# Kernel optimization log

Measured on AMD Instinct MI355X. Metric: run time of the kernel, lower is better.

The kernel has to match this reference:

```python
import jax, jax.numpy as jnp
import numpy as np

R0 = 1.0
N_NODES = 10000
N_EDGES = 160000
DIM_A, DIM_V, DIM_D, CHAN = 64, 32, 16, 16

# Levi-Civita tensor for the antisymmetric (cross-product-like) products
_EPS = np.zeros((3, 3, 3), dtype=np.float32)
for (i, j, k), s in (((0,1,2),1.),((1,2,0),1.),((2,0,1),1.),((0,2,1),-1.),((2,1,0),-1.),((1,0,2),-1.)):
    _EPS[i, j, k] = s


def _tl(W, x):
    """TensLinear: mix channel axis 1 of x (B, din, *(3,)*rank) with W (dout, din)."""
    y = jnp.tensordot(x, W, axes=((1,), (1,)))  # (B, *(3,)*rank, dout)
    return jnp.moveaxis(y, -1, 1)


def radial_encode_8(r, r0):
    # 8 Gaussian radial basis functions on |r|/r0
    d = jnp.linalg.norm(r, axis=-1)            # (E,)
    x = d * (8.0 / r0)
    mu = jnp.arange(8, dtype=r.dtype)
    return jnp.exp(-0.5 * (x[:, None] - mu[None, :]) ** 2)  # (E, 8)


def tens_sigmoid_1(v):
    # equivariant squashing: scale vector by tanh(|v|)/|v|
    n = jnp.linalg.norm(v, axis=-1, keepdims=True)
    return v * jnp.tanh(n) / (n + 1e-12)


def _forward(floats, src, dst, n_nodes):
    (r_ij, x_a, x_v, x_d, W_L0, W_L1, W_L2,
     W_Y000, W_Y110, W_Y220, W_Y011, W_Y101, W_Y121, W_Y211,
     W_Y022, W_Y202, W_Y112, W_Y222, W_Y111, W_Y212,
     W_enc, b_enc, W_dir, W1, b1, W2, b2, W3, b3) = floats
    eps = jnp.asarray(_EPS)
    rad = radial_encode_8(r_ij, R0) @ W_enc.T + b_enc        # (E, chan)
    r = tens_sigmoid_1(r_ij * (7.0 / R0))                    # (E, 3)
    phi_a = rad                                              # (E, chan)
    phi_v = rad[:, :, None] * r[:, None, :]                  # (E, chan, 3)
    phi_d = rad[:, :, None, None] * r[:, None, None, :] * r[:, None, :, None]  # (E, chan, 3, 3)
    # gather destination-node features per edge
    x_a_j = _tl(W_L0, x_a)[dst]                              # (E, chan)
    x_v_j = _tl(W_L1, x_v)[dst]                              # (E, chan, 3)
    x_d_j = _tl(W_L2, x_d)[dst]                              # (E, chan, 3, 3)
    # equivariant tensor products (Bee.apply)
    y_000 = x_a_j * phi_a
    y_110 = jnp.sum(x_v_j * phi_v, -1)
    y_220 = jnp.sum(x_d_j * phi_d, (-2, -1))
    y_011 = x_a_j[..., None] * phi_v
    y_101 = x_v_j * phi_a[..., None]
    y_121 = jnp.einsum('ecj,ecji->eci', x_v_j, phi_d)
    y_211 = jnp.einsum('ecij,ecj->eci', x_d_j, phi_v)
    y_022 = x_a_j[..., None, None] * phi_d
    y_202 = x_d_j * phi_a[..., None, None]
    y_112 = x_v_j[..., :, None] * phi_v[..., None, :]
    y_222 = jnp.einsum('ecik,eckj->ecij', x_d_j, phi_d)
    y_111 = jnp.cross(x_v_j, phi_v)
    y_212 = jnp.einsum('ikl,eckj,ecl->ecij', eps, x_d_j, phi_v)
    psi_a = _tl(W_Y000, y_000) + _tl(W_Y110, y_110) + _tl(W_Y220, y_220)
    psi_v = (_tl(W_Y011, y_011) + _tl(W_Y101, y_101) + _tl(W_Y121, y_121)
             + _tl(W_Y211, y_211) + _tl(W_Y111, y_111))
    psi_d = (_tl(W_Y022, y_022) + _tl(W_Y202, y_202) + _tl(W_Y112, y_112)
             + _tl(W_Y222, y_222) + _tl(W_Y212, y_212))
    # residual MLP on the scalar channel: lin_direct(x) + layers(x)
    lrelu = lambda x: jnp.where(x >= 0, x, 0.1 * x)
    h = lrelu(psi_a @ W1.T + b1)
    h = lrelu(h @ W2.T + b2)
    psi_a = psi_a + psi_a @ W_dir.T + (h @ W3.T + b3)
    # scatter-reduce messages to source nodes
    B_a = jax.ops.segment_sum(psi_a, src, num_segments=n_nodes)
    B_v = jax.ops.segment_sum(psi_v, src, num_segments=n_nodes)
    B_d = jax.ops.segment_sum(psi_d, src, num_segments=n_nodes)
    return 0.1 * B_a, 0.1 * B_v, 0.1 * B_d


def setup_inputs() -> dict:
    key = jax.random.key(0)
    ks = jax.random.split(key, 32)
    f32 = jnp.float32
    nrm = lambda k, shape, scale=1.0: scale * jax.random.normal(k, shape, dtype=f32)
    E, N = N_EDGES, N_NODES
    sC = CHAN ** -0.5
    inp = {
        'r_ij': nrm(ks[0], (E, 3)),
        'x_a': nrm(ks[1], (N, DIM_A)),
        'x_v': nrm(ks[2], (N, DIM_V, 3)),
        'x_d': nrm(ks[3], (N, DIM_D, 3, 3)),
        'W_L0': nrm(ks[4], (CHAN, DIM_A), DIM_A ** -0.5),
        'W_L1': nrm(ks[5], (CHAN, DIM_V), DIM_V ** -0.5),
        'W_L2': nrm(ks[6], (CHAN, DIM_D), DIM_D ** -0.5),
        'W_Y000': nrm(ks[7], (DIM_A, CHAN), sC),
        'W_Y110': nrm(ks[8], (DIM_A, CHAN), sC),
        'W_Y220': nrm(ks[9], (DIM_A, CHAN), sC),
        'W_Y011': nrm(ks[10], (DIM_V, CHAN), sC),
        'W_Y101': nrm(ks[11], (DIM_V, CHAN), sC),
        'W_Y121': nrm(ks[12], (DIM_V, CHAN), sC),
        'W_Y211': nrm(ks[13], (DIM_V, CHAN), sC),
        'W_Y022': nrm(ks[14], (DIM_D, CHAN), sC),
        'W_Y202': nrm(ks[15], (DIM_D, CHAN), sC),
        'W_Y112': nrm(ks[16], (DIM_D, CHAN), sC),
        'W_Y222': nrm(ks[17], (DIM_D, CHAN), sC),
        'W_Y111': nrm(ks[18], (DIM_V, CHAN), sC),
        'W_Y212': nrm(ks[19], (DIM_D, CHAN), sC),
        'W_enc': nrm(ks[20], (CHAN, 8), 8 ** -0.5),
        'b_enc': jnp.zeros((CHAN,), f32),
        'W_dir': nrm(ks[21], (DIM_A, DIM_A), DIM_A ** -0.5),
        'W1': nrm(ks[22], (2 * DIM_A, DIM_A), DIM_A ** -0.5),
        'b1': jnp.zeros((2 * DIM_A,), f32),
        'W2': nrm(ks[23], (2 * DIM_A, 2 * DIM_A), (2 * DIM_A) ** -0.5),
        'b2': jnp.zeros((2 * DIM_A,), f32),
        'W3': nrm(ks[24], (DIM_A, 2 * DIM_A), (2 * DIM_A) ** -0.5),
        'b3': jnp.zeros((DIM_A,), f32),
        'src': jax.random.randint(ks[25], (E,), 0, N, dtype=jnp.int32),
        'dst': jax.random.randint(ks[26], (E,), 0, N, dtype=jnp.int32),
        'n_nodes': N,
    }
    return inp


def reference(r_ij, x_a, x_v, x_d, W_L0, W_L1, W_L2, W_Y000, W_Y110, W_Y220,
              W_Y011, W_Y101, W_Y121, W_Y211, W_Y022, W_Y202, W_Y112, W_Y222,
              W_Y111, W_Y212, W_enc, b_enc, W_dir, W1, b1, W2, b2, W3, b3,
              src, dst, n_nodes):
    floats = (r_ij, x_a, x_v, x_d, W_L0, W_L1, W_L2, W_Y000, W_Y110, W_Y220,
              W_Y011, W_Y101, W_Y121, W_Y211, W_Y022, W_Y202, W_Y112, W_Y222,
              W_Y111, W_Y212, W_enc, b_enc, W_dir, W1, b1, W2, b2, W3, b3)
    return _forward(floats, src, dst, n_nodes)
```

## Files before the change

kernel.cpp:

```cpp
#include <hip/hip_runtime.h>
#include <hip/hip_bf16.h>

typedef __hip_bfloat16 bf16;
typedef __attribute__((ext_vector_type(8))) short bf16x8;
typedef __attribute__((ext_vector_type(4))) float f32x4;

__device__ __forceinline__ void st_bf16(short* p, float v) {
    uint32_t u = __float_as_uint(v) + 0x8000u;
    *p = (short)(u >> 16);
}
__device__ __forceinline__ float bb2f(short s) {
    uint32_t u = ((uint32_t)(uint16_t)s) << 16;
    return __uint_as_float(u);
}

__global__ __launch_bounds__(256) void prep_all(
    const float* __restrict__ W000, const float* __restrict__ W110, const float* __restrict__ W220,
    const float* __restrict__ W011, const float* __restrict__ W101, const float* __restrict__ W121,
    const float* __restrict__ W211, const float* __restrict__ W111,
    const float* __restrict__ W022, const float* __restrict__ W202, const float* __restrict__ W112,
    const float* __restrict__ W222, const float* __restrict__ W212,
    const float* __restrict__ W1, const float* __restrict__ W2, const float* __restrict__ W3,
    const float* __restrict__ Wdir, bf16* __restrict__ wout,
    const float* __restrict__ xa, const float* __restrict__ xv, const float* __restrict__ xd,
    const float* __restrict__ WL0, const float* __restrict__ WL1, const float* __restrict__ WL2,
    float* __restrict__ Pa, float* __restrict__ Pv, float* __restrict__ Pd, int N, int NPB,
    const int* __restrict__ src, const int* __restrict__ dst,
    int* __restrict__ cnt_s, int* __restrict__ cnt_d, int E)
{
    int b = blockIdx.x;
    const int tid = threadIdx.x;
    if (b < 178) {
        int i = b * 256 + tid;
        if (i >= 45568) return;
        float v = 0.f;
        if (i < 4096) {
            int o = i >> 6, k = i & 63;
            if (k < 48) {
                int t = k >> 4, c = k & 15;
                const float* W = (t == 0) ? W000 : (t == 1) ? W110 : W220;
                v = W[o * 16 + c];
            }
        } else if (i < 7168) {
            int r = i - 4096, ch = r / 96, k = r % 96;
            if (k < 80) {
                int t = k >> 4, c = k & 15;
                const float* W = (t == 0) ? W011 : (t == 1) ? W101 : (t == 2) ? W121 : (t == 3) ? W211 : W111;
                v = W[ch * 16 + c];
            }
        } else if (i < 8704) {
            int r = i - 7168, ch = r / 96, k = r % 96;
            if (k < 80) {
                int t = k >> 4, c = k & 15;
                const float* W = (t == 0) ? W022 : (t == 1) ? W202 : (t == 2) ? W112 : (t == 3) ? W222 : W212;
                v = W[ch * 16 + c];
            }
        } else if (i < 16896) v = W1[i - 8704];
        else if (i < 33280) v = W2[i - 16896];
        else if (i < 41472) v = W3[i - 33280];
        else v = Wdir[i - 41472];
        wout[i] = __float2bfloat16(v);
        return;
    }
    b -= 178;
    if (b < NPB) {
        __shared__ float sxa[256], sxv[384], sxd[576];
        const int n0 = b * 4;
        if (n0 + tid / 64 < N) sxa[tid] = xa[(size_t)n0 * 64 + tid];
        for (int i = tid; i < 384; i += 256) if (n0 + i / 96 < N)  sxv[i] = xv[(size_t)n0 * 96 + i];
        for (int i = tid; i < 576; i += 256) if (n0 + i / 144 < N) sxd[i] = xd[(size_t)n0 * 144 + i];
        __syncthreads();
        for (int o = tid; o < 832; o += 256) {
            int ln = o / 208, s = o % 208;
            int n = n0 + ln;
            if (n >= N) continue;
            if (s < 16) {
                float a = 0.f;
                const float* w = WL0 + s * 64;
                const float* x = sxa + ln * 64;
                for (int d = 0; d < 64; ++d) a += w[d] * x[d];
                Pa[(size_t)n * 16 + s] = a;
            } else if (s < 64) {
                int idx = s - 16, c = idx / 3, i = idx % 3;
                float a = 0.f;
                const float* w = WL1 + c * 32;
                const float* x = sxv + ln * 96;
                for (int d = 0; d < 32; ++d) a += w[d] * x[d * 3 + i];
                Pv[(size_t)n * 64 + c * 4 + i] = a;
            } else {
                int idx = s - 64, c = idx / 9, ij = idx % 9;
                float a = 0.f;
                const float* w = WL2 + c * 16;
                const float* x = sxd + ln * 144;
                for (int d = 0; d < 16; ++d) a += w[d] * x[d * 9 + ij];
                Pd[(size_t)n * 192 + c * 12 + ij] = a;
            }
        }
        return;
    }
    b -= NPB;
    int i = b * 256 + tid;
    if (i < E) {
        atomicAdd(&cnt_s[src[i]], 1);
        atomicAdd(&cnt_d[dst[i]], 1);
    }
}

__global__ void scan_rows2(const int* __restrict__ cnt_s, int* __restrict__ rs_s,
                           const int* __restrict__ cnt_d, int* __restrict__ rs_d, int N) {
    const int* cnt = blockIdx.x ? cnt_d : cnt_s;
    int* rowstart = blockIdx.x ? rs_d : rs_s;
    __shared__ int ps[256];
    int t = threadIdx.x;
    int chunk = (N + 255) / 256;
    int base = t * chunk;
    int s = 0;
    for (int i = 0; i < chunk; ++i) { int idx = base + i; if (idx < N) s += cnt[idx]; }
    ps[t] = s;
    __syncthreads();
    for (int off = 1; off < 256; off <<= 1) {
        int v = (t >= off) ? ps[t - off] : 0;
        __syncthreads();
        ps[t] += v;
        __syncthreads();
    }
    int run = (t > 0) ? ps[t - 1] : 0;
    for (int i = 0; i < chunk; ++i) {
        int idx = base + i;
        if (idx < N) { rowstart[idx] = run; run += cnt[idx]; }
    }
    if (t == 255) rowstart[N] = run;
}

__global__ void fill_slot(const int* __restrict__ src, const int* __restrict__ dst,
                          const int* __restrict__ rs_s, const int* __restrict__ rs_d,
                          int* __restrict__ cur_s, int* __restrict__ cur_d,
                          int* __restrict__ slot, int* __restrict__ eperm, int E) {
    int i = blockIdx.x * 256 + threadIdx.x;
    if (i < E) {
        slot[i] = rs_s[src[i]] + atomicAdd(&cur_s[src[i]], 1);
        int p = rs_d[dst[i]] + atomicAdd(&cur_d[dst[i]], 1);
        eperm[p] = i;
    }
}

__global__ __launch_bounds__(256) void edge_mfma(
    const float* __restrict__ r_ij,
    const float* __restrict__ Pa, const float* __restrict__ Pv, const float* __restrict__ Pd,
    const float* __restrict__ Wenc, const float* __restrict__ benc,
    const bf16* __restrict__ Wa, const bf16* __restrict__ Wv, const bf16* __restrict__ Wd,
    const bf16* __restrict__ Wb1, const bf16* __restrict__ Wb2,
    const bf16* __restrict__ Wb3, const bf16* __restrict__ Wbdir,
    const float* __restrict__ b1, const float* __restrict__ b2, const float* __restrict__ b3,
    const int* __restrict__ slot, const int* __restrict__ dst,
    const int* __restrict__ eperm,
    short* __restrict__ psi, int E, int nwg)
{
    __shared__ __align__(16) char smem[32320];
    short* SYA   = (short*)smem;
    short* SYV   = (short*)(smem + 1536);
    short* SYD   = (short*)(smem + 9216);
    int*   SSLOT = (int*)(smem + 32256);
    short* SPSIA = (short*)(smem + 1536);
    short* SH1   = (short*)(smem + 3840);
    short* SH2   = (short*)(smem + 8192);
    short* SPSI  = (short*)(smem + 12544);

    const int tid = threadIdx.x;
    int orig = blockIdx.x;
    int q = nwg >> 3, r = nwg & 7;
    int xcd = orig & 7, idx = orig >> 3;
    int tile = (xcd < r) ? (xcd * (q + 1) + idx) : (r * (q + 1) + (xcd - r) * q + idx);
    const int e0 = tile * 16;
    const bf16x8 z8 = {};

    {
        const int le = tid >> 4, c = tid & 15;
        if (e0 + le < E) {
            const int e = eperm[e0 + le];
            const int j = dst[e];
            if (c == 0) SSLOT[le] = slot[e];
            float vx = 7.f * r_ij[e * 3 + 0];
            float vy = 7.f * r_ij[e * 3 + 1];
            float vz = 7.f * r_ij[e * 3 + 2];
            float nn = sqrtf(vx * vx + vy * vy + vz * vz);
            float ex = __expf(-2.f * nn);
            float th = (1.f - ex) * __builtin_amdgcn_rcpf(1.f + ex);
            float sc = th * __builtin_amdgcn_rcpf(nn + 1e-12f);
            float rr[3] = {vx * sc, vy * sc, vz * sc};
            float x8 = nn * (8.f / 7.f);
            float rad = benc[c];
            #pragma unroll
            for (int m = 0; m < 8; ++m) {
                float tt = x8 - (float)m;
                rad += __expf(-0.5f * tt * tt) * Wenc[c * 8 + m];
            }
            float xa = Pa[j * 16 + c];
            f32x4 pv4 = *(const f32x4*)(Pv + (size_t)j * 64 + c * 4);
            f32x4 pd0 = *(const f32x4*)(Pd + (size_t)j * 192 + c * 12);
            f32x4 pd1 = *(const f32x4*)(Pd + (size_t)j * 192 + c * 12 + 4);
            f32x4 pd2 = *(const f32x4*)(Pd + (size_t)j * 192 + c * 12 + 8);
            float xv[3] = {pv4[0], pv4[1], pv4[2]};
            float xd[9] = {pd0[0], pd0[1], pd0[2], pd0[3], pd1[0], pd1[1], pd1[2], pd1[3], pd2[0]};
            float dotv = xv[0] * rr[0] + xv[1] * rr[1] + xv[2] * rr[2];
            float mv[3];
            #pragma unroll
            for (int i = 0; i < 3; ++i)
                mv[i] = xd[i * 3] * rr[0] + xd[i * 3 + 1] * rr[1] + xd[i * 3 + 2] * rr[2];
            float quad = mv[0] * rr[0] + mv[1] * rr[1] + mv[2] * rr[2];
            st_bf16(&SYA[le * 48 + c],      xa * rad);
            st_bf16(&SYA[le * 48 + 16 + c], rad * dotv);
            st_bf16(&SYA[le * 48 + 32 + c], rad * quad);
            #pragma unroll
            for (int i = 0; i < 3; ++i) {
                int row = (le * 3 + i) * 80;
                int i1 = (i + 1) % 3, i2 = (i + 2) % 3;
                st_bf16(&SYV[row + c],      xa * rad * rr[i]);
                st_bf16(&SYV[row + 16 + c], rad * xv[i]);
                st_bf16(&SYV[row + 32 + c], rad * dotv * rr[i]);
                st_bf16(&SYV[row + 48 + c], rad * mv[i]);
                st_bf16(&SYV[row + 64 + c], rad * (xv[i1] * rr[i2] - xv[i2] * rr[i1]));
            }
            #pragma unroll
            for (int i = 0; i < 3; ++i) {
                int i1 = (i + 1) % 3, i2 = (i + 2) % 3;
                #pragma unroll
                for (int jj = 0; jj < 3; ++jj) {
                    int row = (le * 9 + i * 3 + jj) * 80;
                    st_bf16(&SYD[row + c],      xa * rad * rr[i] * rr[jj]);
                    st_bf16(&SYD[row + 16 + c], rad * xd[i * 3 + jj]);
                    st_bf16(&SYD[row + 32 + c], rad * xv[i] * rr[jj]);
                    st_bf16(&SYD[row + 48 + c], rad * mv[i] * rr[jj]);
                    st_bf16(&SYD[row + 64 + c], rad * (xd[i1 * 3 + jj] * rr[i2] - xd[i2 * 3 + jj] * rr[i1]));
                }
            }
        }
    }
    __syncthreads();

    const int wid = tid >> 6, lane = tid & 63;
    const int q16 = lane >> 4, r16 = lane & 15;

    f32x4 da[4] = {};
    f32x4 dv[3][2] = {};
    f32x4 dd[5] = {};
    const int mstart = (wid == 2) ? 0 : 5;
    const int mcnt = (wid == 2) ? 5 : 4;

    if (wid == 0) {
        bf16x8 af0 = *(const bf16x8*)&SYA[r16 * 48 + q16 * 8];
        bf16x8 af1 = z8;
        if (q16 < 2) af1 = *(const bf16x8*)&SYA[r16 * 48 + 32 + q16 * 8];
        #pragma unroll
        for (int n = 0; n < 4; ++n) {
            bf16x8 bf0 = *(const bf16x8*)((const short*)Wa + (n * 16 + r16) * 64 + q16 * 8);
            bf16x8 bf1 = *(const bf16x8*)((const short*)Wa + (n * 16 + r16) * 64 + 32 + q16 * 8);
            da[n] = __builtin_amdgcn_mfma_f32_16x16x32_bf16(af0, bf0, da[n], 0, 0, 0);
            da[n] = __builtin_amdgcn_mfma_f32_16x16x32_bf16(af1, bf1, da[n], 0, 0, 0);
        }
    } else if (wid == 1) {
        #pragma unroll
        for (int ks = 0; ks < 3; ++ks) {
            bf16x8 av[3], bv[2];
            #pragma unroll
            for (int m = 0; m < 3; ++m) {
                if (ks < 2) av[m] = *(const bf16x8*)&SYV[(m * 16 + r16) * 80 + ks * 32 + q16 * 8];
                else {
                    av[m] = z8;
                    if (q16 < 2) av[m] = *(const bf16x8*)&SYV[(m * 16 + r16) * 80 + 64 + q16 * 8];
                }
            }
            #pragma unroll
            for (int n = 0; n < 2; ++n)
                bv[n] = *(const bf16x8*)((const short*)Wv + (n * 16 + r16) * 96 + ks * 32 + q16 * 8);
            #pragma unroll
            for (int m = 0; m < 3; ++m)
                #pragma unroll
                for (int n = 0; n < 2; ++n)
                    dv[m][n] = __builtin_amdgcn_mfma_f32_16x16x32_bf16(av[m], bv[n], dv[m][n], 0, 0, 0);
        }
    } else {
        #pragma unroll
        for (int ks = 0; ks < 3; ++ks) {
            bf16x8 bf = *(const bf16x8*)((const short*)Wd + r16 * 96 + ks * 32 + q16 * 8);
            for (int mi = 0; mi < mcnt; ++mi) {
                bf16x8 af;
                if (ks < 2) af = *(const bf16x8*)&SYD[((mstart + mi) * 16 + r16) * 80 + ks * 32 + q16 * 8];
                else {
                    af = z8;
                    if (q16 < 2) af = *(const bf16x8*)&SYD[((mstart + mi) * 16 + r16) * 80 + 64 + q16 * 8];
                }
                dd[mi] = __builtin_amdgcn_mfma_f32_16x16x32_bf16(af, bf, dd[mi], 0, 0, 0);
            }
        }
    }
    __syncthreads();

    if (wid == 0) {
        #pragma unroll
        for (int n = 0; n < 4; ++n)
            #pragma unroll
            for (int jj = 0; jj < 4; ++jj)
                st_bf16(&SPSIA[(q16 * 4 + jj) * 72 + n * 16 + r16], da[n][jj]);
    } else if (wid == 1) {
        #pragma unroll
        for (int m = 0; m < 3; ++m)
            #pragma unroll
            for (int n = 0; n < 2; ++n)
                #pragma unroll
                for (int jj = 0; jj < 4; ++jj) {
                    int row = m * 16 + q16 * 4 + jj;
                    int el = row / 3, i = row % 3;
                    st_bf16(&SPSI[el * 304 + 64 + (n * 16 + r16) * 3 + i], dv[m][n][jj]);
                }
    } else {
        for (int mi = 0; mi < mcnt; ++mi)
            #pragma unroll
            for (int jj = 0; jj < 4; ++jj) {
                int row = (mstart + mi) * 16 + q16 * 4 + jj;
                int el = row / 9, ij = row % 9;
                st_bf16(&SPSI[el * 304 + 160 + r16 * 9 + ij], dd[mi][jj]);
            }
    }
    __syncthreads();

    {
        f32x4 h1a[2] = {};
        #pragma unroll
        for (int ks = 0; ks < 2; ++ks) {
            bf16x8 af = *(const bf16x8*)&SPSIA[r16 * 72 + ks * 32 + q16 * 8];
            #pragma unroll
            for (int n = 0; n < 2; ++n) {
                int col = wid * 32 + n * 16 + r16;
                bf16x8 bf = *(const bf16x8*)((const short*)Wb1 + col * 64 + ks * 32 + q16 * 8);
                h1a[n] = __builtin_amdgcn_mfma_f32_16x16x32_bf16(af, bf, h1a[n], 0, 0, 0);
            }
        }
        #pragma unroll
        for (int n = 0; n < 2; ++n) {
            int col = wid * 32 + n * 16 + r16;
            float bias = b1[col];
            #pragma unroll
            for (int jj = 0; jj < 4; ++jj) {
                float v = h1a[n][jj] + bias;
                v = v >= 0.f ? v : 0.1f * v;
                st_bf16(&SH1[(q16 * 4 + jj) * 136 + col], v);
            }
        }
    }
    __syncthreads();
    {
        f32x4 h2a[2] = {};
        #pragma unroll
        for (int ks = 0; ks < 4; ++ks) {
            bf16x8 af = *(const bf16x8*)&SH1[r16 * 136 + ks * 32 + q16 * 8];
            #pragma unroll
            for (int n = 0; n < 2; ++n) {
                int col = wid * 32 + n * 16 + r16;
                bf16x8 bf = *(const bf16x8*)((const short*)Wb2 + col * 128 + ks * 32 + q16 * 8);
                h2a[n] = __builtin_amdgcn_mfma_f32_16x16x32_bf16(af, bf, h2a[n], 0, 0, 0);
            }
        }
        #pragma unroll
        for (int n = 0; n < 2; ++n) {
            int col = wid * 32 + n * 16 + r16;
            float bias = b2[col];
            #pragma unroll
            for (int jj = 0; jj < 4; ++jj) {
                float v = h2a[n][jj] + bias;
                v = v >= 0.f ? v : 0.1f * v;
                st_bf16(&SH2[(q16 * 4 + jj) * 136 + col], v);
            }
        }
    }
    __syncthreads();
    {
        f32x4 o3 = {};
        const int col3 = wid * 16 + r16;
        #pragma unroll
        for (int ks = 0; ks < 4; ++ks) {
            bf16x8 af = *(const bf16x8*)&SH2[r16 * 136 + ks * 32 + q16 * 8];
            bf16x8 bf = *(const bf16x8*)((const short*)Wb3 + col3 * 128 + ks * 32 + q16 * 8);
            o3 = __builtin_amdgcn_mfma_f32_16x16x32_bf16(af, bf, o3, 0, 0, 0);
        }
        #pragma unroll
        for (int ks = 0; ks < 2; ++ks) {
            bf16x8 af = *(const bf16x8*)&SPSIA[r16 * 72 + ks * 32 + q16 * 8];
            bf16x8 bf = *(const bf16x8*)((const short*)Wbdir + col3 * 64 + ks * 32 + q16 * 8);
            o3 = __builtin_amdgcn_mfma_f32_16x16x32_bf16(af, bf, o3, 0, 0, 0);
        }
        float bias = b3[col3];
        #pragma unroll
        for (int jj = 0; jj < 4; ++jj) {
            int row = q16 * 4 + jj;
            float v = o3[jj] + bias + bb2f(SPSIA[row * 72 + col3]);
            st_bf16(&SPSI[row * 304 + col3], v);
        }
    }
    __syncthreads();

    {
        const uint32_t* S32 = (const uint32_t*)SPSI;
        uint32_t* P32 = (uint32_t*)psi;
        for (int idx2 = tid; idx2 < 16 * 152; idx2 += 256) {
            int le = idx2 / 152, k = idx2 - le * 152;
            if (e0 + le < E)
                P32[(size_t)SSLOT[le] * 152 + k] = S32[le * 152 + k];
        }
    }
}

__global__ __launch_bounds__(128) void gather(
    const short* __restrict__ psi, const int* __restrict__ rowstart,
    float* __restrict__ out, int N) {
    int n = blockIdx.x, t = threadIdx.x;
    if (t >= 76) return;
    int s0 = rowstart[n], s1 = rowstart[n + 1];
    float a0 = 0.f, a1 = 0.f, a2 = 0.f, a3 = 0.f;
    for (int s = s0; s < s1; ++s) {
        const uint32_t* p = (const uint32_t*)(psi + (size_t)s * 304) + 2 * t;
        uint32_t u0 = p[0], u1 = p[1];
        a0 += __uint_as_float(u0 << 16);
        a1 += __uint_as_float(u0 & 0xffff0000u);
        a2 += __uint_as_float(u1 << 16);
        a3 += __uint_as_float(u1 & 0xffff0000u);
    }
    int f = 4 * t;
    f32x4 v = {0.1f * a0, 0.1f * a1, 0.1f * a2, 0.1f * a3};
    if (f < 64)       *(f32x4*)&out[(size_t)n * 64 + f] = v;
    else if (f < 160) *(f32x4*)&out[(size_t)N * 64 + (size_t)n * 96 + (f - 64)] = v;
    else              *(f32x4*)&out[(size_t)N * 160 + (size_t)n * 144 + (f - 160)] = v;
}

extern "C" void kernel_launch(void* const* d_in, const int* in_sizes, int n_in,
                              void* d_out, int out_size, void* d_ws, size_t ws_size,
                              hipStream_t stream) {
    const float* r_ij = (const float*)d_in[0];
    const float* x_a  = (const float*)d_in[1];
    const float* x_v  = (const float*)d_in[2];
    const float* x_d  = (const float*)d_in[3];
    const float* W_L0 = (const float*)d_in[4];
    const float* W_L1 = (const float*)d_in[5];
    const float* W_L2 = (const float*)d_in[6];
    const float* W000 = (const float*)d_in[7];
    const float* W110 = (const float*)d_in[8];
    const float* W220 = (const float*)d_in[9];
    const float* W011 = (const float*)d_in[10];
    const float* W101 = (const float*)d_in[11];
    const float* W121 = (const float*)d_in[12];
    const float* W211 = (const float*)d_in[13];
    const float* W022 = (const float*)d_in[14];
    const float* W202 = (const float*)d_in[15];
    const float* W112 = (const float*)d_in[16];
    const float* W222 = (const float*)d_in[17];
    const float* W111 = (const float*)d_in[18];
    const float* W212 = (const float*)d_in[19];
    const float* Wenc = (const float*)d_in[20];
    const float* benc = (const float*)d_in[21];
    const float* Wdir = (const float*)d_in[22];
    const float* W1   = (const float*)d_in[23];
    const float* b1   = (const float*)d_in[24];
    const float* W2   = (const float*)d_in[25];
    const float* b2   = (const float*)d_in[26];
    const float* W3   = (const float*)d_in[27];
    const float* b3   = (const float*)d_in[28];
    const int* src    = (const int*)d_in[29];
    const int* dst    = (const int*)d_in[30];

    const int E = in_sizes[29];
    const int N = in_sizes[1] / 64;

    float* Pa     = (float*)d_ws;
    float* Pv     = Pa + (size_t)N * 16;
    float* Pd     = Pv + (size_t)N * 64;
    bf16*  Wb     = (bf16*)(Pd + (size_t)N * 192);
    int*   cnt_s  = (int*)(Wb + 45568);
    int*   cur_s  = cnt_s + N;
    int*   cnt_d  = cur_s + N;
    int*   cur_d  = cnt_d + N;
    int*   rs_s   = cur_d + N;
    int*   rs_d   = rs_s + N + 1;
    int*   slot   = rs_d + N + 1;
    int*   eperm  = slot + E;
    short* psi    = (short*)(eperm + E);

    const bf16* Wa_p    = Wb;
    const bf16* Wv_p    = Wb + 4096;
    const bf16* Wd_p    = Wb + 7168;
    const bf16* Wb1_p   = Wb + 8704;
    const bf16* Wb2_p   = Wb + 16896;
    const bf16* Wb3_p   = Wb + 33280;
    const bf16* Wbdir_p = Wb + 41472;

    const int NPB = (N + 3) / 4;
    const int HB  = (E + 255) / 256;
    const int nwg = (E + 15) / 16;

    hipMemsetAsync(cnt_s, 0, (size_t)4 * N * sizeof(int), stream);
    prep_all<<<178 + NPB + HB, 256, 0, stream>>>(
        W000, W110, W220, W011, W101, W121, W211, W111,
        W022, W202, W112, W222, W212, W1, W2, W3, Wdir, Wb,
        x_a, x_v, x_d, W_L0, W_L1, W_L2, Pa, Pv, Pd, N, NPB,
        src, dst, cnt_s, cnt_d, E);
    scan_rows2<<<2, 256, 0, stream>>>(cnt_s, rs_s, cnt_d, rs_d, N);
    fill_slot<<<HB, 256, 0, stream>>>(src, dst, rs_s, rs_d, cur_s, cur_d, slot, eperm, E);
    edge_mfma<<<nwg, 256, 0, stream>>>(
        r_ij, Pa, Pv, Pd, Wenc, benc,
        Wa_p, Wv_p, Wd_p, Wb1_p, Wb2_p, Wb3_p, Wbdir_p,
        b1, b2, b3, slot, dst, eperm, psi, E, nwg);
    gather<<<N, 128, 0, stream>>>(psi, rs_s, (float*)d_out, N);
}
```

Baseline: 253.9 us.

## Drop dst-sorted edge permutation and fill_slot kernel; assign slots inside edge kernel

```diff
diff --git a/kernel.cpp b/kernel.cpp
--- a/kernel.cpp
+++ b/kernel.cpp
@@ -25,8 +25,7 @@
     const float* __restrict__ xa, const float* __restrict__ xv, const float* __restrict__ xd,
     const float* __restrict__ WL0, const float* __restrict__ WL1, const float* __restrict__ WL2,
     float* __restrict__ Pa, float* __restrict__ Pv, float* __restrict__ Pd, int N, int NPB,
-    const int* __restrict__ src, const int* __restrict__ dst,
-    int* __restrict__ cnt_s, int* __restrict__ cnt_d, int E)
+    const int* __restrict__ src, int* __restrict__ cnt, int E)
 {
     int b = blockIdx.x;
     const int tid = threadIdx.x;
@@ -100,16 +99,10 @@
     }
     b -= NPB;
     int i = b * 256 + tid;
-    if (i < E) {
-        atomicAdd(&cnt_s[src[i]], 1);
-        atomicAdd(&cnt_d[dst[i]], 1);
-    }
-}
-
-__global__ void scan_rows2(const int* __restrict__ cnt_s, int* __restrict__ rs_s,
-                           const int* __restrict__ cnt_d, int* __restrict__ rs_d, int N) {
-    const int* cnt = blockIdx.x ? cnt_d : cnt_s;
-    int* rowstart = blockIdx.x ? rs_d : rs_s;
+    if (i < E) atomicAdd(&cnt[src[i]], 1);
+}
+
+__global__ void scan_rows(const int* __restrict__ cnt, int* __restrict__ rowstart, int N) {
     __shared__ int ps[256];
     int t = threadIdx.x;
     int chunk = (N + 255) / 256;
@@ -130,18 +123,6 @@
         if (idx < N) { rowstart[idx] = run; run += cnt[idx]; }
     }
     if (t == 255) rowstart[N] = run;
-}
-
-__global__ void fill_slot(const int* __restrict__ src, const int* __restrict__ dst,
-                          const int* __restrict__ rs_s, const int* __restrict__ rs_d,
-                          int* __restrict__ cur_s, int* __restrict__ cur_d,
-                          int* __restrict__ slot, int* __restrict__ eperm, int E) {
-    int i = blockIdx.x * 256 + threadIdx.x;
-    if (i < E) {
-        slot[i] = rs_s[src[i]] + atomicAdd(&cur_s[src[i]], 1);
-        int p = rs_d[dst[i]] + atomicAdd(&cur_d[dst[i]], 1);
-        eperm[p] = i;
-    }
 }
 
 __global__ __launch_bounds__(256) void edge_mfma(
@@ -152,9 +133,9 @@
     const bf16* __restrict__ Wb1, const bf16* __restrict__ Wb2,
     const bf16* __restrict__ Wb3, const bf16* __restrict__ Wbdir,
     const float* __restrict__ b1, const float* __restrict__ b2, const float* __restrict__ b3,
-    const int* __restrict__ slot, const int* __restrict__ dst,
-    const int* __restrict__ eperm,
-    short* __restrict__ psi, int E, int nwg)
+    const int* __restrict__ src, const int* __restrict__ dst,
+    const int* __restrict__ rs, int* __restrict__ cur,
+    short* __restrict__ psi, int E)
 {
     __shared__ __align__(16) char smem[32320];
     short* SYA   = (short*)smem;
@@ -167,19 +148,15 @@
     short* SPSI  = (short*)(smem + 12544);
 
     const int tid = threadIdx.x;
-    int orig = blockIdx.x;
-    int q = nwg >> 3, r = nwg & 7;
-    int xcd = orig & 7, idx = orig >> 3;
-    int tile = (xcd < r) ? (xcd * (q + 1) + idx) : (r * (q + 1) + (xcd - r) * q + idx);
-    const int e0 = tile * 16;
+    const int e0 = blockIdx.x * 16;
     const bf16x8 z8 = {};
 
     {
         const int le = tid >> 4, c = tid & 15;
-        if (e0 + le < E) {
-            const int e = eperm[e0 + le];
+        const int e = e0 + le;
+        if (e < E) {
             const int j = dst[e];
-            if (c == 0) SSLOT[le] = slot[e];
+            if (c == 0) SSLOT[le] = rs[src[e]] + atomicAdd(&cur[src[e]], 1);
             float vx = 7.f * r_ij[e * 3 + 0];
             float vy = 7.f * r_ij[e * 3 + 1];
             float vz = 7.f * r_ij[e * 3 + 2];
@@ -474,15 +451,10 @@
     float* Pv     = Pa + (size_t)N * 16;
     float* Pd     = Pv + (size_t)N * 64;
     bf16*  Wb     = (bf16*)(Pd + (size_t)N * 192);
-    int*   cnt_s  = (int*)(Wb + 45568);
-    int*   cur_s  = cnt_s + N;
-    int*   cnt_d  = cur_s + N;
-    int*   cur_d  = cnt_d + N;
-    int*   rs_s   = cur_d + N;
-    int*   rs_d   = rs_s + N + 1;
-    int*   slot   = rs_d + N + 1;
-    int*   eperm  = slot + E;
-    short* psi    = (short*)(eperm + E);
+    int*   cnt    = (int*)(Wb + 45568);
+    int*   cur    = cnt + N;
+    int*   rs     = cur + N;
+    short* psi    = (short*)(rs + N + 1);
 
     const bf16* Wa_p    = Wb;
     const bf16* Wv_p    = Wb + 4096;
@@ -494,19 +466,17 @@
 
     const int NPB = (N + 3) / 4;
     const int HB  = (E + 255) / 256;
-    const int nwg = (E + 15) / 16;
-
-    hipMemsetAsync(cnt_s, 0, (size_t)4 * N * sizeof(int), stream);
+
+    hipMemsetAsync(cnt, 0, (size_t)2 * N * sizeof(int), stream);
     prep_all<<<178 + NPB + HB, 256, 0, stream>>>(
         W000, W110, W220, W011, W101, W121, W211, W111,
         W022, W202, W112, W222, W212, W1, W2, W3, Wdir, Wb,
         x_a, x_v, x_d, W_L0, W_L1, W_L2, Pa, Pv, Pd, N, NPB,
-        src, dst, cnt_s, cnt_d, E);
-    scan_rows2<<<2, 256, 0, stream>>>(cnt_s, rs_s, cnt_d, rs_d, N);
-    fill_slot<<<HB, 256, 0, stream>>>(src, dst, rs_s, rs_d, cur_s, cur_d, slot, eperm, E);
-    edge_mfma<<<nwg, 256, 0, stream>>>(
+        src, cnt, E);
+    scan_rows<<<1, 256, 0, stream>>>(cnt, rs, N);
+    edge_mfma<<<(E + 15) / 16, 256, 0, stream>>>(
         r_ij, Pa, Pv, Pd, Wenc, benc,
         Wa_p, Wv_p, Wd_p, Wb1_p, Wb2_p, Wb3_p, Wbdir_p,
-        b1, b2, b3, slot, dst, eperm, psi, E, nwg);
-    gather<<<N, 128, 0, stream>>>(psi, rs_s, (float*)d_out, N);
-}
+        b1, b2, b3, src, dst, rs, cur, psi, E);
+    gather<<<N, 128, 0, stream>>>(psi, rs, (float*)d_out, N);
+}
```

Result: faster. 230.1 us (-9.4%).
